# Kernel tuning notes

Hardware: AMD Instinct MI355X
Metric: run time of the kernel (lower is better)

The kernel has to match this reference:

```python
import jax, jax.numpy as jnp
import numpy as np

IN_DIM = 512
OUT_DIM = 512
KEY_DIM = 512
FILTER_LENGTH = 32
STRIDE = 4
B, T = 8, 2048


def setup_inputs() -> dict:
    key = jax.random.key(0)
    ks = jax.random.split(key, 7)
    s_in = 1.0 / np.sqrt(IN_DIM)
    x = jax.random.normal(ks[0], (B, T, IN_DIM), dtype=jnp.float32)
    Wq = jax.random.uniform(ks[1], (IN_DIM, KEY_DIM), jnp.float32, -s_in, s_in)
    bq = jax.random.uniform(ks[2], (KEY_DIM,), jnp.float32, -s_in, s_in)
    Wk = jax.random.uniform(ks[3], (IN_DIM, KEY_DIM), jnp.float32, -s_in, s_in)
    bk = jax.random.uniform(ks[4], (KEY_DIM,), jnp.float32, -s_in, s_in)
    Wv = jax.random.uniform(ks[5], (IN_DIM, OUT_DIM), jnp.float32, -s_in, s_in)
    bv = jax.random.uniform(ks[6], (OUT_DIM,), jnp.float32, -s_in, s_in)
    return {"x": x, "Wq": Wq, "bq": bq, "Wk": Wk, "bk": bk, "Wv": Wv, "bv": bv}


def reference(x, Wq, bq, Wk, bk, Wv, bv):
    # x: (B, T, in_dim)
    Bsz, T_, _ = x.shape
    F = FILTER_LENGTH
    T_out = (T_ - F) // STRIDE + 1
    starts = jnp.arange(T_out) * STRIDE                 # (T_out,)
    win_idx = starts[:, None] + jnp.arange(F)[None, :]  # (T_out, F)
    center_idx = starts + F // 2                        # (T_out,)

    q = x @ Wq + bq   # (B, T, key_dim)
    k = x @ Wk + bk   # (B, T, key_dim)
    v = x @ Wv + bv   # (B, T, out_dim)

    q_c = q[:, center_idx]    # (B, T_out, key_dim) query at window center
    k_w = k[:, win_idx]       # (B, T_out, F, key_dim)
    v_w = v[:, win_idx]       # (B, T_out, F, out_dim)

    scale = 1.0 / jnp.sqrt(jnp.asarray(KEY_DIM, dtype=q.dtype))
    scores = jnp.einsum('btd,btfd->btf', q_c, k_w) * scale  # (B, T_out, F)
    attn = jax.nn.softmax(scores, axis=-1)
    out = jnp.einsum('btf,btfd->btd', attn, v_w)            # (B, T_out, out_dim)
    return out
```

## Files before the change

### kernel.cpp

```cpp
#include <hip/hip_runtime.h>
#include <hip/hip_bf16.h>
#include <cstdint>

#define FLT 32
#define TOUT 505
#define TT 2048
#define MROWS 16384
#define QROWS 4040
#define KDIM 512
#define BK 64
#define NT 8

typedef float f32x4 __attribute__((ext_vector_type(4)));
typedef __bf16 bf16x8 __attribute__((ext_vector_type(8)));

static __device__ __forceinline__ ushort f2bf(float f) {
  uint32_t u = __float_as_uint(f);
  uint32_t r = (u + 0x7fffu + ((u >> 16) & 1u)) >> 16;
  return (ushort)r;
}
static __device__ __forceinline__ float bf2f(ushort h) {
  return __uint_as_float(((uint32_t)h) << 16);
}
static __device__ __forceinline__ void pack8(const float4& lo, const float4& hi, ushort* v8) {
  v8[0] = f2bf(lo.x); v8[1] = f2bf(lo.y); v8[2] = f2bf(lo.z); v8[3] = f2bf(lo.w);
  v8[4] = f2bf(hi.x); v8[5] = f2bf(hi.y); v8[6] = f2bf(hi.z); v8[7] = f2bf(hi.w);
}

__global__ void wprep_kernel(const float* __restrict__ Wq, const float* __restrict__ Wk,
                             const float* __restrict__ Wv, const float* __restrict__ bq,
                             const float* __restrict__ bk, const float* __restrict__ bv,
                             ushort* __restrict__ wt, float* __restrict__ bias) {
  const int bid = blockIdx.x;
  const int tid = threadIdx.x;
  if (bid < 192) {
    __shared__ ushort lds[64][66];
    int mat = bid >> 6;
    int w = bid & 63;
    int k0 = (w >> 3) * 64, n0 = (w & 7) * 64;
    const float* W = (mat == 0) ? Wq : (mat == 1) ? Wk : Wv;
    int nn = tid & 63;
    #pragma unroll
    for (int r = 0; r < 16; ++r) {
      int kk = r * 4 + (tid >> 6);
      lds[kk][nn] = f2bf(W[(size_t)(k0 + kk) * 512 + n0 + nn]);
    }
    __syncthreads();
    int kk2 = tid & 63;
    #pragma unroll
    for (int r = 0; r < 16; ++r) {
      int nn2 = r * 4 + (tid >> 6);
      wt[(size_t)(mat * 512 + n0 + nn2) * 512 + k0 + kk2] = lds[kk2][nn2];
    }
  } else {
    #pragma unroll
    for (int e = 0; e < 6; ++e) {
      int n = tid * 6 + e;
      const float* bsrc = (n < 512) ? bq : (n < 1024) ? bk : bv;
      bias[n] = bsrc[n & 511];
    }
  }
}

__global__ __launch_bounds__(256, 2) void gemm_kernel(
    const float* __restrict__ xf, const ushort* __restrict__ wt,
    const float* __restrict__ bias, ushort* __restrict__ kv, ushort* __restrict__ qc) {
  __shared__ char smem[33792];
  ushort* const As = (ushort*)smem;
  ushort* const Bs = (ushort*)(smem + 16384);

  const int tid = threadIdx.x;
  const int lane = tid & 63;
  const int wv = tid >> 6;
  const int bid = blockIdx.x;

  int m0, n0, ost, gather, mlim;
  const ushort* wtb;
  const float* biasb;
  ushort* outp;
  if (bid < 1024) {
    int swz = (bid & 7) * 128 + (bid >> 3);
    m0 = (swz >> 3) * 128; n0 = (swz & 7) * 128;
    wtb = wt + (size_t)512 * KDIM; biasb = bias + 512;
    outp = kv; ost = 1024; gather = 0; mlim = MROWS;
  } else {
    int b2 = bid - 1024;
    int swz = (b2 & 7) * 16 + (b2 >> 3);
    m0 = (swz >> 2) * 128; n0 = (swz & 3) * 128;
    wtb = wt; biasb = bias;
    outp = qc; ost = 512; gather = 1; mlim = QROWS;
  }

  const float* aF[4];
  uint aDst[4];
  const ushort* bS[4];
  #pragma unroll
  for (int i = 0; i < 4; ++i) {
    int idx = i * 4096 + tid * 16;
    int row = idx >> 7;
    int colb = idx & 127;
    aDst[i] = (uint)(row * 128 + (colb ^ ((row & 7) << 4)));
    int scol = (colb ^ ((row & 7) << 4)) >> 1;
    size_t arow;
    if (gather) {
      int r = m0 + row;
      if (r > QROWS - 1) r = QROWS - 1;
      int bb = r / TOUT;
      int t2 = r - bb * TOUT;
      arow = (size_t)bb * TT + (size_t)t2 * 4 + FLT / 2;
    } else {
      arow = (size_t)(m0 + row);
    }
    aF[i] = xf + arow * KDIM + (colb >> 1);
    bS[i] = wtb + (size_t)(n0 + row) * KDIM + scol;
  }

  const int fr = lane & 15;
  const int fq = lane >> 4;
  const int wr = wv >> 1;
  const int wc = wv & 1;

  f32x4 acc[4][4];
  #pragma unroll
  for (int i = 0; i < 4; ++i)
    #pragma unroll
    for (int j = 0; j < 4; ++j) acc[i][j] = (f32x4){0.f, 0.f, 0.f, 0.f};

  for (int t = 0; t < NT; ++t) {
    __syncthreads();
    const int koff = t * BK;
    #pragma unroll
    for (int i = 0; i < 4; ++i) {
      __builtin_amdgcn_global_load_lds(
          (const __attribute__((address_space(1))) unsigned int*)(bS[i] + koff),
          (__attribute__((address_space(3))) unsigned int*)((char*)Bs + i * 4096 + tid * 16),
          16, 0, 0);
    }
    #pragma unroll
    for (int i = 0; i < 4; ++i) {
      float4 lo = *reinterpret_cast<const float4*>(aF[i] + koff);
      float4 hi = *reinterpret_cast<const float4*>(aF[i] + koff + 4);
      ushort v8[8]; pack8(lo, hi, v8);
      *reinterpret_cast<uint4*>((char*)As + aDst[i]) = *reinterpret_cast<const uint4*>(v8);
    }
    __syncthreads();

    #pragma unroll
    for (int ks = 0; ks < 2; ++ks) {
      bf16x8 af[4], bg[4];
      #pragma unroll
      for (int i = 0; i < 4; ++i) {
        int ra = wr * 64 + i * 16 + fr;
        int ca = ks * 64 + fq * 16;
        af[i] = *reinterpret_cast<const bf16x8*>(
            (const char*)As + ra * 128 + (ca ^ ((ra & 7) << 4)));
        int rb = wc * 64 + i * 16 + fr;
        bg[i] = *reinterpret_cast<const bf16x8*>(
            (const char*)Bs + rb * 128 + (ca ^ ((rb & 7) << 4)));
      }
      #pragma unroll
      for (int i = 0; i < 4; ++i)
        #pragma unroll
        for (int j = 0; j < 4; ++j)
          acc[i][j] = __builtin_amdgcn_mfma_f32_16x16x32_bf16(af[i], bg[j], acc[i][j], 0, 0, 0);
    }
  }

  __syncthreads();
  ushort* const ep = (ushort*)smem;
  #pragma unroll
  for (int j = 0; j < 4; ++j) {
    int colg = n0 + wc * 64 + j * 16 + fr;
    int coll = wc * 64 + j * 16 + fr;
    float bvl = biasb[colg];
    #pragma unroll
    for (int i = 0; i < 4; ++i) {
      int rowl = wr * 64 + i * 16 + fq * 4;
      #pragma unroll
      for (int r = 0; r < 4; ++r)
        ep[(rowl + r) * 132 + coll] = f2bf(acc[i][j][r] + bvl);
    }
  }
  __syncthreads();
  #pragma unroll
  for (int it = 0; it < 8; ++it) {
    int row = it * 16 + (tid >> 4);
    int gr = m0 + row;
    if (gr < mlim) {
      uint4 val = *reinterpret_cast<const uint4*>(&ep[row * 132 + (tid & 15) * 8]);
      *reinterpret_cast<uint4*>(outp + (size_t)gr * ost + n0 + (tid & 15) * 8) = val;
    }
  }
}

__global__ __launch_bounds__(256) void attn_kernel(
    const ushort* __restrict__ kv,
    const ushort* __restrict__ qc,
    float* __restrict__ out) {
  __shared__ float q_lds[KDIM];
  __shared__ float s_lds[FLT];
  __shared__ float p_lds[FLT];

  const int bid = blockIdx.x;
  const int b = bid & 7;
  const int t = bid >> 3;
  const size_t base_row = (size_t)b * TT + (size_t)t * 4;
  const int tid = threadIdx.x;
  const int lane = tid & 63;
  const int wv = tid >> 6;

  {
    const ushort* qrow = qc + ((size_t)b * TOUT + t) * KDIM;
    uint v = *reinterpret_cast<const uint*>(qrow + tid * 2);
    q_lds[tid * 2]     = bf2f((ushort)(v & 0xffffu));
    q_lds[tid * 2 + 1] = bf2f((ushort)(v >> 16));
  }
  __syncthreads();

  const int fl = lane >> 3;
  const int f = wv * 8 + fl;
  const int sub = lane & 7;
  const ushort* krow = kv + (base_row + f) * 1024;
  float acc = 0.f;
  #pragma unroll
  for (int j = 0; j < 8; ++j) {
    int d = (j * 8 + sub) * 8;
    uint4 kv4 = *reinterpret_cast<const uint4*>(krow + d);
    const ushort* ks = reinterpret_cast<const ushort*>(&kv4);
    #pragma unroll
    for (int e = 0; e < 8; ++e) acc += q_lds[d + e] * bf2f(ks[e]);
  }
  acc += __shfl_xor(acc, 1);
  acc += __shfl_xor(acc, 2);
  acc += __shfl_xor(acc, 4);
  if (sub == 0) s_lds[f] = acc * 0.04419417382415922f;
  __syncthreads();

  float m = -1e30f;
  #pragma unroll
  for (int i = 0; i < FLT; ++i) m = fmaxf(m, s_lds[i]);
  if (tid < FLT) p_lds[tid] = __expf(s_lds[tid] - m);
  __syncthreads();
  float sum = 0.f;
  #pragma unroll
  for (int i = 0; i < FLT; ++i) sum += p_lds[i];
  const float inv = 1.f / sum;

  const int d = tid * 2;
  float o0 = 0.f, o1 = 0.f;
  const ushort* vbase = kv + base_row * 1024 + 512 + d;
  #pragma unroll
  for (int ff = 0; ff < FLT; ++ff) {
    uint vvv = *reinterpret_cast<const uint*>(vbase + (size_t)ff * 1024);
    float w = p_lds[ff] * inv;
    o0 += w * bf2f((ushort)(vvv & 0xffffu));
    o1 += w * bf2f((ushort)(vvv >> 16));
  }
  float2* op = reinterpret_cast<float2*>(out + ((size_t)b * TOUT + t) * 512 + d);
  *op = make_float2(o0, o1);
}

extern "C" void kernel_launch(void* const* d_in, const int* in_sizes, int n_in,
                              void* d_out, int out_size, void* d_ws, size_t ws_size,
                              hipStream_t stream) {
  const float* x  = (const float*)d_in[0];
  const float* Wq = (const float*)d_in[1];
  const float* bq = (const float*)d_in[2];
  const float* Wk = (const float*)d_in[3];
  const float* bk = (const float*)d_in[4];
  const float* Wv = (const float*)d_in[5];
  const float* bv = (const float*)d_in[6];
  float* out = (float*)d_out;

  char* ws = (char*)d_ws;
  ushort* wt   = (ushort*)ws;
  float*  bias = (float*)(ws + 1572864);
  ushort* kvb  = (ushort*)(ws + 1581056);
  ushort* qc   = (ushort*)(ws + 1581056 + 33554432);

  hipLaunchKernelGGL(wprep_kernel, dim3(193), dim3(256), 0, stream,
                     Wq, Wk, Wv, bq, bk, bv, wt, bias);
  hipLaunchKernelGGL(gemm_kernel, dim3(1152), dim3(256), 0, stream,
                     x, wt, bias, kvb, qc);
  hipLaunchKernelGGL(attn_kernel, dim3(QROWS), dim3(256), 0, stream, kvb, qc, out);
}
```

Measured before the change: 60.25 us.

## Load A fragments directly from global into registers, drop A LDS staging

The GEMM no longer stages the fp32-to-bf16 converted A tile in shared memory. Each wave loads its own A fragment straight from global memory into registers and converts it with native bf16 casts. The LDS-staged epilogue is replaced by direct scattered 2-byte global stores, and launch bounds are raised to allow more blocks per CU. This cuts LDS usage and sync work, but A rows are now re-read by both column waves, global A loads are less coalesced, and the output stores are narrow and uncoalesced.

```diff
diff --git a/kernel.cpp b/kernel.cpp
--- a/kernel.cpp
+++ b/kernel.cpp
@@ -22,9 +22,11 @@
 static __device__ __forceinline__ float bf2f(ushort h) {
   return __uint_as_float(((uint32_t)h) << 16);
 }
-static __device__ __forceinline__ void pack8(const float4& lo, const float4& hi, ushort* v8) {
-  v8[0] = f2bf(lo.x); v8[1] = f2bf(lo.y); v8[2] = f2bf(lo.z); v8[3] = f2bf(lo.w);
-  v8[4] = f2bf(hi.x); v8[5] = f2bf(hi.y); v8[6] = f2bf(hi.z); v8[7] = f2bf(hi.w);
+static __device__ __forceinline__ bf16x8 cvt8(const float4& lo, const float4& hi) {
+  bf16x8 v;
+  v[0] = (__bf16)lo.x; v[1] = (__bf16)lo.y; v[2] = (__bf16)lo.z; v[3] = (__bf16)lo.w;
+  v[4] = (__bf16)hi.x; v[5] = (__bf16)hi.y; v[6] = (__bf16)hi.z; v[7] = (__bf16)hi.w;
+  return v;
 }
 
 __global__ void wprep_kernel(const float* __restrict__ Wq, const float* __restrict__ Wk,
@@ -62,19 +64,17 @@
   }
 }
 
-__global__ __launch_bounds__(256, 2) void gemm_kernel(
+__global__ __launch_bounds__(256, 4) void gemm_kernel(
     const float* __restrict__ xf, const ushort* __restrict__ wt,
     const float* __restrict__ bias, ushort* __restrict__ kv, ushort* __restrict__ qc) {
-  __shared__ char smem[33792];
-  ushort* const As = (ushort*)smem;
-  ushort* const Bs = (ushort*)(smem + 16384);
+  __shared__ ushort Bs[128 * 64];
 
   const int tid = threadIdx.x;
   const int lane = tid & 63;
   const int wv = tid >> 6;
   const int bid = blockIdx.x;
 
-  int m0, n0, ost, gather, mlim;
+  int m0, n0, ost, gather;
   const ushort* wtb;
   const float* biasb;
   ushort* outp;
@@ -82,43 +82,45 @@
     int swz = (bid & 7) * 128 + (bid >> 3);
     m0 = (swz >> 3) * 128; n0 = (swz & 7) * 128;
     wtb = wt + (size_t)512 * KDIM; biasb = bias + 512;
-    outp = kv; ost = 1024; gather = 0; mlim = MROWS;
+    outp = kv; ost = 1024; gather = 0;
   } else {
     int b2 = bid - 1024;
     int swz = (b2 & 7) * 16 + (b2 >> 3);
     m0 = (swz >> 2) * 128; n0 = (swz & 3) * 128;
     wtb = wt; biasb = bias;
-    outp = qc; ost = 512; gather = 1; mlim = QROWS;
-  }
-
-  const float* aF[4];
-  uint aDst[4];
+    outp = qc; ost = 512; gather = 1;
+  }
+
   const ushort* bS[4];
   #pragma unroll
   for (int i = 0; i < 4; ++i) {
     int idx = i * 4096 + tid * 16;
     int row = idx >> 7;
     int colb = idx & 127;
-    aDst[i] = (uint)(row * 128 + (colb ^ ((row & 7) << 4)));
     int scol = (colb ^ ((row & 7) << 4)) >> 1;
+    bS[i] = wtb + (size_t)(n0 + row) * KDIM + scol;
+  }
+
+  const int fr = lane & 15;
+  const int fq = lane >> 4;
+  const int wr = wv >> 1;
+  const int wc = wv & 1;
+
+  const float* aP[4];
+  #pragma unroll
+  for (int i = 0; i < 4; ++i) {
+    int r = m0 + wr * 64 + i * 16 + fr;
     size_t arow;
     if (gather) {
-      int r = m0 + row;
       if (r > QROWS - 1) r = QROWS - 1;
       int bb = r / TOUT;
       int t2 = r - bb * TOUT;
       arow = (size_t)bb * TT + (size_t)t2 * 4 + FLT / 2;
     } else {
-      arow = (size_t)(m0 + row);
-    }
-    aF[i] = xf + arow * KDIM + (colb >> 1);
-    bS[i] = wtb + (size_t)(n0 + row) * KDIM + scol;
-  }
-
-  const int fr = lane & 15;
-  const int fq = lane >> 4;
-  const int wr = wv >> 1;
-  const int wc = wv & 1;
+      arow = (size_t)r;
+    }
+    aP[i] = xf + arow * KDIM;
+  }
 
   f32x4 acc[4][4];
   #pragma unroll
@@ -136,26 +138,24 @@
           (__attribute__((address_space(3))) unsigned int*)((char*)Bs + i * 4096 + tid * 16),
           16, 0, 0);
     }
-    #pragma unroll
-    for (int i = 0; i < 4; ++i) {
-      float4 lo = *reinterpret_cast<const float4*>(aF[i] + koff);
-      float4 hi = *reinterpret_cast<const float4*>(aF[i] + koff + 4);
-      ushort v8[8]; pack8(lo, hi, v8);
-      *reinterpret_cast<uint4*>((char*)As + aDst[i]) = *reinterpret_cast<const uint4*>(v8);
-    }
     __syncthreads();
 
     #pragma unroll
     for (int ks = 0; ks < 2; ++ks) {
-      bf16x8 af[4], bg[4];
+      bf16x8 af[4];
       #pragma unroll
       for (int i = 0; i < 4; ++i) {
-        int ra = wr * 64 + i * 16 + fr;
+        const float* p = aP[i] + koff + ks * 32 + fq * 8;
+        float4 lo = *reinterpret_cast<const float4*>(p);
+        float4 hi = *reinterpret_cast<const float4*>(p + 4);
+        af[i] = cvt8(lo, hi);
+      }
+      bf16x8 bg[4];
+      #pragma unroll
+      for (int j = 0; j < 4; ++j) {
+        int rb = wc * 64 + j * 16 + fr;
         int ca = ks * 64 + fq * 16;
-        af[i] = *reinterpret_cast<const bf16x8*>(
-            (const char*)As + ra * 128 + (ca ^ ((ra & 7) << 4)));
-        int rb = wc * 64 + i * 16 + fr;
-        bg[i] = *reinterpret_cast<const bf16x8*>(
+        bg[j] = *reinterpret_cast<const bf16x8*>(
             (const char*)Bs + rb * 128 + (ca ^ ((rb & 7) << 4)));
       }
       #pragma unroll
@@ -166,29 +166,18 @@
     }
   }
 
-  __syncthreads();
-  ushort* const ep = (ushort*)smem;
   #pragma unroll
   for (int j = 0; j < 4; ++j) {
-    int colg = n0 + wc * 64 + j * 16 + fr;
-    int coll = wc * 64 + j * 16 + fr;
-    float bvl = biasb[colg];
+    int col = n0 + wc * 64 + j * 16 + fr;
+    float bvl = biasb[col];
     #pragma unroll
     for (int i = 0; i < 4; ++i) {
-      int rowl = wr * 64 + i * 16 + fq * 4;
-      #pragma unroll
-      for (int r = 0; r < 4; ++r)
-        ep[(rowl + r) * 132 + coll] = f2bf(acc[i][j][r] + bvl);
-    }
-  }
-  __syncthreads();
-  #pragma unroll
-  for (int it = 0; it < 8; ++it) {
-    int row = it * 16 + (tid >> 4);
-    int gr = m0 + row;
-    if (gr < mlim) {
-      uint4 val = *reinterpret_cast<const uint4*>(&ep[row * 132 + (tid & 15) * 8]);
-      *reinterpret_cast<uint4*>(outp + (size_t)gr * ost + n0 + (tid & 15) * 8) = val;
+      int rowb = m0 + wr * 64 + i * 16 + fq * 4;
+      #pragma unroll
+      for (int r = 0; r < 4; ++r) {
+        if (!gather || (rowb + r) < QROWS)
+          outp[(size_t)(rowb + r) * ost + col] = f2bf(acc[i][j][r] + bvl);
+      }
     }
   }
 }
```

Result: slower. 136.5 us (+126.5%).

## Apply attention weights to x and project with Wv afterwards; drop key bias

Applied to the files above, without the earlier changes.

Since the softmax weights sum to one, attn·(xWv+bv) equals (attn·x)Wv+bv, so V is no longer materialised for all rows. The key bias is dropped because it shifts every score in a window by the same amount and cancels in softmax. The attention kernel now stages a bf16 window of x in LDS for 8 consecutive outputs and writes a weighted-x buffer, and a new small GEMM applies Wv plus bias. This removes the large V projection and the K/V writes, at the cost of an extra kernel launch, fewer and larger attention blocks (512 instead of 4040), and an extra bf16 rounding of the intermediate.

```diff
diff --git a/kernel.cpp b/kernel.cpp
--- a/kernel.cpp
+++ b/kernel.cpp
@@ -28,43 +28,32 @@
 }
 
 __global__ void wprep_kernel(const float* __restrict__ Wq, const float* __restrict__ Wk,
-                             const float* __restrict__ Wv, const float* __restrict__ bq,
-                             const float* __restrict__ bk, const float* __restrict__ bv,
-                             ushort* __restrict__ wt, float* __restrict__ bias) {
+                             const float* __restrict__ Wv, ushort* __restrict__ wt) {
   const int bid = blockIdx.x;
   const int tid = threadIdx.x;
-  if (bid < 192) {
-    __shared__ ushort lds[64][66];
-    int mat = bid >> 6;
-    int w = bid & 63;
-    int k0 = (w >> 3) * 64, n0 = (w & 7) * 64;
-    const float* W = (mat == 0) ? Wq : (mat == 1) ? Wk : Wv;
-    int nn = tid & 63;
-    #pragma unroll
-    for (int r = 0; r < 16; ++r) {
-      int kk = r * 4 + (tid >> 6);
-      lds[kk][nn] = f2bf(W[(size_t)(k0 + kk) * 512 + n0 + nn]);
-    }
-    __syncthreads();
-    int kk2 = tid & 63;
-    #pragma unroll
-    for (int r = 0; r < 16; ++r) {
-      int nn2 = r * 4 + (tid >> 6);
-      wt[(size_t)(mat * 512 + n0 + nn2) * 512 + k0 + kk2] = lds[kk2][nn2];
-    }
-  } else {
-    #pragma unroll
-    for (int e = 0; e < 6; ++e) {
-      int n = tid * 6 + e;
-      const float* bsrc = (n < 512) ? bq : (n < 1024) ? bk : bv;
-      bias[n] = bsrc[n & 511];
-    }
+  __shared__ ushort lds[64][66];
+  int mat = bid >> 6;
+  int w = bid & 63;
+  int k0 = (w >> 3) * 64, n0 = (w & 7) * 64;
+  const float* W = (mat == 0) ? Wq : (mat == 1) ? Wk : Wv;
+  int nn = tid & 63;
+  #pragma unroll
+  for (int r = 0; r < 16; ++r) {
+    int kk = r * 4 + (tid >> 6);
+    lds[kk][nn] = f2bf(W[(size_t)(k0 + kk) * 512 + n0 + nn]);
+  }
+  __syncthreads();
+  int kk2 = tid & 63;
+  #pragma unroll
+  for (int r = 0; r < 16; ++r) {
+    int nn2 = r * 4 + (tid >> 6);
+    wt[(size_t)(mat * 512 + n0 + nn2) * 512 + k0 + kk2] = lds[kk2][nn2];
   }
 }
 
 __global__ __launch_bounds__(256, 2) void gemm_kernel(
     const float* __restrict__ xf, const ushort* __restrict__ wt,
-    const float* __restrict__ bias, ushort* __restrict__ kv, ushort* __restrict__ qc) {
+    const float* __restrict__ bq, ushort* __restrict__ kb, ushort* __restrict__ qc) {
   __shared__ char smem[33792];
   ushort* const As = (ushort*)smem;
   ushort* const Bs = (ushort*)(smem + 16384);
@@ -74,21 +63,20 @@
   const int wv = tid >> 6;
   const int bid = blockIdx.x;
 
-  int m0, n0, ost, gather, mlim;
+  int m0, n0, gather, mlim;
   const ushort* wtb;
-  const float* biasb;
   ushort* outp;
-  if (bid < 1024) {
-    int swz = (bid & 7) * 128 + (bid >> 3);
-    m0 = (swz >> 3) * 128; n0 = (swz & 7) * 128;
-    wtb = wt + (size_t)512 * KDIM; biasb = bias + 512;
-    outp = kv; ost = 1024; gather = 0; mlim = MROWS;
+  if (bid < 512) {
+    int swz = (bid & 7) * 64 + (bid >> 3);
+    m0 = (swz >> 2) * 128; n0 = (swz & 3) * 128;
+    wtb = wt + (size_t)512 * KDIM;
+    outp = kb; gather = 0; mlim = MROWS;
   } else {
-    int b2 = bid - 1024;
+    int b2 = bid - 512;
     int swz = (b2 & 7) * 16 + (b2 >> 3);
     m0 = (swz >> 2) * 128; n0 = (swz & 3) * 128;
-    wtb = wt; biasb = bias;
-    outp = qc; ost = 512; gather = 1; mlim = QROWS;
+    wtb = wt;
+    outp = qc; gather = 1; mlim = QROWS;
   }
 
   const float* aF[4];
@@ -170,9 +158,9 @@
   ushort* const ep = (ushort*)smem;
   #pragma unroll
   for (int j = 0; j < 4; ++j) {
-    int colg = n0 + wc * 64 + j * 16 + fr;
+    int col = n0 + wc * 64 + j * 16 + fr;
     int coll = wc * 64 + j * 16 + fr;
-    float bvl = biasb[colg];
+    float bvl = gather ? bq[col] : 0.f;
     #pragma unroll
     for (int i = 0; i < 4; ++i) {
       int rowl = wr * 64 + i * 16 + fq * 4;
@@ -188,76 +176,190 @@
     int gr = m0 + row;
     if (gr < mlim) {
       uint4 val = *reinterpret_cast<const uint4*>(&ep[row * 132 + (tid & 15) * 8]);
-      *reinterpret_cast<uint4*>(outp + (size_t)gr * ost + n0 + (tid & 15) * 8) = val;
+      *reinterpret_cast<uint4*>(outp + (size_t)gr * 512 + n0 + (tid & 15) * 8) = val;
     }
   }
 }
 
 __global__ __launch_bounds__(256) void attn_kernel(
-    const ushort* __restrict__ kv,
+    const float* __restrict__ xf,
+    const ushort* __restrict__ kb,
     const ushort* __restrict__ qc,
-    float* __restrict__ out) {
-  __shared__ float q_lds[KDIM];
+    ushort* __restrict__ ubuf) {
+  __shared__ char xw[61440];
+  __shared__ float q_lds[512];
   __shared__ float s_lds[FLT];
   __shared__ float p_lds[FLT];
 
   const int bid = blockIdx.x;
   const int b = bid & 7;
-  const int t = bid >> 3;
-  const size_t base_row = (size_t)b * TT + (size_t)t * 4;
+  const int g = bid >> 3;
+  const int t0 = g * 8;
+  const int nt = min(8, TOUT - t0);
+  const int rows = 4 * (nt - 1) + 32;
+  const size_t base_row = (size_t)b * TT + (size_t)t0 * 4;
   const int tid = threadIdx.x;
   const int lane = tid & 63;
   const int wv = tid >> 6;
 
-  {
-    const ushort* qrow = qc + ((size_t)b * TOUT + t) * KDIM;
-    uint v = *reinterpret_cast<const uint*>(qrow + tid * 2);
-    q_lds[tid * 2]     = bf2f((ushort)(v & 0xffffu));
-    q_lds[tid * 2 + 1] = bf2f((ushort)(v >> 16));
-  }
-  __syncthreads();
-
-  const int fl = lane >> 3;
-  const int f = wv * 8 + fl;
-  const int sub = lane & 7;
-  const ushort* krow = kv + (base_row + f) * 1024;
-  float acc = 0.f;
-  #pragma unroll
-  for (int j = 0; j < 8; ++j) {
-    int d = (j * 8 + sub) * 8;
-    uint4 kv4 = *reinterpret_cast<const uint4*>(krow + d);
-    const ushort* ks = reinterpret_cast<const ushort*>(&kv4);
-    #pragma unroll
-    for (int e = 0; e < 8; ++e) acc += q_lds[d + e] * bf2f(ks[e]);
-  }
-  acc += __shfl_xor(acc, 1);
-  acc += __shfl_xor(acc, 2);
-  acc += __shfl_xor(acc, 4);
-  if (sub == 0) s_lds[f] = acc * 0.04419417382415922f;
-  __syncthreads();
-
-  float m = -1e30f;
-  #pragma unroll
-  for (int i = 0; i < FLT; ++i) m = fmaxf(m, s_lds[i]);
-  if (tid < FLT) p_lds[tid] = __expf(s_lds[tid] - m);
-  __syncthreads();
-  float sum = 0.f;
-  #pragma unroll
-  for (int i = 0; i < FLT; ++i) sum += p_lds[i];
-  const float inv = 1.f / sum;
-
-  const int d = tid * 2;
-  float o0 = 0.f, o1 = 0.f;
-  const ushort* vbase = kv + base_row * 1024 + 512 + d;
-  #pragma unroll
-  for (int ff = 0; ff < FLT; ++ff) {
-    uint vvv = *reinterpret_cast<const uint*>(vbase + (size_t)ff * 1024);
-    float w = p_lds[ff] * inv;
-    o0 += w * bf2f((ushort)(vvv & 0xffffu));
-    o1 += w * bf2f((ushort)(vvv >> 16));
-  }
-  float2* op = reinterpret_cast<float2*>(out + ((size_t)b * TOUT + t) * 512 + d);
-  *op = make_float2(o0, o1);
+  #pragma unroll
+  for (int i = 0; i < 15; ++i) {
+    int gi = i * 2048 + tid * 8;
+    int row = gi >> 9;
+    int col = gi & 511;
+    if (row < rows) {
+      const float* src = xf + (base_row + row) * 512 + col;
+      float4 lo = *reinterpret_cast<const float4*>(src);
+      float4 hi = *reinterpret_cast<const float4*>(src + 4);
+      ushort v8[8]; pack8(lo, hi, v8);
+      *reinterpret_cast<uint4*>(xw + row * 1024 + ((2 * col) ^ ((row & 7) << 4))) =
+          *reinterpret_cast<const uint4*>(v8);
+    }
+  }
+
+  for (int tt = 0; tt < nt; ++tt) {
+    {
+      uint v = *reinterpret_cast<const uint*>(
+          qc + ((size_t)b * TOUT + t0 + tt) * 512 + tid * 2);
+      q_lds[tid * 2]     = bf2f((ushort)(v & 0xffffu));
+      q_lds[tid * 2 + 1] = bf2f((ushort)(v >> 16));
+    }
+    __syncthreads();
+
+    const int f = wv * 8 + (lane >> 3);
+    const int sub = lane & 7;
+    const ushort* krow = kb + (base_row + (size_t)(4 * tt + f)) * 512;
+    float acc = 0.f;
+    #pragma unroll
+    for (int j = 0; j < 8; ++j) {
+      int d = (j * 8 + sub) * 8;
+      uint4 kv4 = *reinterpret_cast<const uint4*>(krow + d);
+      const ushort* ks = reinterpret_cast<const ushort*>(&kv4);
+      #pragma unroll
+      for (int e = 0; e < 8; ++e) acc += q_lds[d + e] * bf2f(ks[e]);
+    }
+    acc += __shfl_xor(acc, 1);
+    acc += __shfl_xor(acc, 2);
+    acc += __shfl_xor(acc, 4);
+    if (sub == 0) s_lds[f] = acc * 0.04419417382415922f;
+    __syncthreads();
+
+    float m = -1e30f;
+    #pragma unroll
+    for (int i2 = 0; i2 < FLT; ++i2) m = fmaxf(m, s_lds[i2]);
+    if (tid < FLT) p_lds[tid] = __expf(s_lds[tid] - m);
+    __syncthreads();
+    float sum = 0.f;
+    #pragma unroll
+    for (int i2 = 0; i2 < FLT; ++i2) sum += p_lds[i2];
+    const float inv = 1.f / sum;
+
+    const int d = tid * 2;
+    float o0 = 0.f, o1 = 0.f;
+    #pragma unroll
+    for (int ff = 0; ff < FLT; ++ff) {
+      int r2 = 4 * tt + ff;
+      uint vv = *reinterpret_cast<const uint*>(
+          xw + r2 * 1024 + ((2 * d) ^ ((r2 & 7) << 4)));
+      float w = p_lds[ff] * inv;
+      o0 += w * bf2f((ushort)(vv & 0xffffu));
+      o1 += w * bf2f((ushort)(vv >> 16));
+    }
+    uint pk = ((uint)f2bf(o1) << 16) | (uint)f2bf(o0);
+    *reinterpret_cast<uint*>(ubuf + ((size_t)b * TOUT + t0 + tt) * 512 + d) = pk;
+    __syncthreads();
+  }
+}
+
+__global__ __launch_bounds__(256, 2) void ogemm_kernel(
+    const ushort* __restrict__ ubuf, const ushort* __restrict__ wvt,
+    const float* __restrict__ bv, float* __restrict__ out) {
+  __shared__ ushort As[128 * 64];
+  __shared__ ushort Bs[128 * 64];
+
+  const int tid = threadIdx.x;
+  const int lane = tid & 63;
+  const int wv = tid >> 6;
+  const int swz = (blockIdx.x & 7) * 16 + (blockIdx.x >> 3);
+  const int m0 = (swz >> 2) * 128;
+  const int n0 = (swz & 3) * 128;
+
+  const ushort* aS[4];
+  const ushort* bS[4];
+  #pragma unroll
+  for (int i = 0; i < 4; ++i) {
+    int idx = i * 4096 + tid * 16;
+    int row = idx >> 7;
+    int colb = idx & 127;
+    int scol = (colb ^ ((row & 7) << 4)) >> 1;
+    int r = m0 + row; if (r > QROWS - 1) r = QROWS - 1;
+    aS[i] = ubuf + (size_t)r * KDIM + scol;
+    bS[i] = wvt + (size_t)(n0 + row) * KDIM + scol;
+  }
+
+  const int fr = lane & 15;
+  const int fq = lane >> 4;
+  const int wr = wv >> 1;
+  const int wc = wv & 1;
+
+  f32x4 acc[4][4];
+  #pragma unroll
+  for (int i = 0; i < 4; ++i)
+    #pragma unroll
+    for (int j = 0; j < 4; ++j) acc[i][j] = (f32x4){0.f, 0.f, 0.f, 0.f};
+
+  for (int t = 0; t < NT; ++t) {
+    __syncthreads();
+    const int koff = t * BK;
+    #pragma unroll
+    for (int i = 0; i < 4; ++i) {
+      int ldst = i * 4096 + tid * 16;
+      __builtin_amdgcn_global_load_lds(
+          (const __attribute__((address_space(1))) unsigned int*)(aS[i] + koff),
+          (__attribute__((address_space(3))) unsigned int*)((char*)As + ldst),
+          16, 0, 0);
+      __builtin_amdgcn_global_load_lds(
+          (const __attribute__((address_space(1))) unsigned int*)(bS[i] + koff),
+          (__attribute__((address_space(3))) unsigned int*)((char*)Bs + ldst),
+          16, 0, 0);
+    }
+    __syncthreads();
+
+    #pragma unroll
+    for (int ks = 0; ks < 2; ++ks) {
+      bf16x8 af[4], bg[4];
+      #pragma unroll
+      for (int i = 0; i < 4; ++i) {
+        int ra = wr * 64 + i * 16 + fr;
+        int ca = ks * 64 + fq * 16;
+        af[i] = *reinterpret_cast<const bf16x8*>(
+            (const char*)As + ra * 128 + (ca ^ ((ra & 7) << 4)));
+        int rb = wc * 64 + i * 16 + fr;
+        bg[i] = *reinterpret_cast<const bf16x8*>(
+            (const char*)Bs + rb * 128 + (ca ^ ((rb & 7) << 4)));
+      }
+      #pragma unroll
+      for (int i = 0; i < 4; ++i)
+        #pragma unroll
+        for (int j = 0; j < 4; ++j)
+          acc[i][j] = __builtin_amdgcn_mfma_f32_16x16x32_bf16(af[i], bg[j], acc[i][j], 0, 0, 0);
+    }
+  }
+
+  #pragma unroll
+  for (int j = 0; j < 4; ++j) {
+    int col = n0 + wc * 64 + j * 16 + fr;
+    float bvl = bv[col];
+    #pragma unroll
+    for (int i = 0; i < 4; ++i) {
+      int rowb = m0 + wr * 64 + i * 16 + fq * 4;
+      #pragma unroll
+      for (int r = 0; r < 4; ++r) {
+        if (rowb + r < QROWS)
+          out[(size_t)(rowb + r) * 512 + col] = acc[i][j][r] + bvl;
+      }
+    }
+  }
 }
 
 extern "C" void kernel_launch(void* const* d_in, const int* in_sizes, int n_in,
@@ -267,20 +369,21 @@
   const float* Wq = (const float*)d_in[1];
   const float* bq = (const float*)d_in[2];
   const float* Wk = (const float*)d_in[3];
-  const float* bk = (const float*)d_in[4];
   const float* Wv = (const float*)d_in[5];
   const float* bv = (const float*)d_in[6];
   float* out = (float*)d_out;
 
   char* ws = (char*)d_ws;
   ushort* wt   = (ushort*)ws;
-  float*  bias = (float*)(ws + 1572864);
-  ushort* kvb  = (ushort*)(ws + 1581056);
-  ushort* qc   = (ushort*)(ws + 1581056 + 33554432);
-
-  hipLaunchKernelGGL(wprep_kernel, dim3(193), dim3(256), 0, stream,
-                     Wq, Wk, Wv, bq, bk, bv, wt, bias);
-  hipLaunchKernelGGL(gemm_kernel, dim3(1152), dim3(256), 0, stream,
-                     x, wt, bias, kvb, qc);
-  hipLaunchKernelGGL(attn_kernel, dim3(QROWS), dim3(256), 0, stream, kvb, qc, out);
-}
+  ushort* kb   = (ushort*)(ws + 1572864);
+  ushort* qc   = (ushort*)(ws + 1572864 + 16777216);
+  ushort* ubuf = (ushort*)(ws + 1572864 + 16777216 + 4194304);
+
+  hipLaunchKernelGGL(wprep_kernel, dim3(192), dim3(256), 0, stream, Wq, Wk, Wv, wt);
+  hipLaunchKernelGGL(gemm_kernel, dim3(640), dim3(256), 0, stream,
+                     x, wt, bq, kb, qc);
+  hipLaunchKernelGGL(attn_kernel, dim3(512), dim3(256), 0, stream,
+                     x, kb, qc, ubuf);
+  hipLaunchKernelGGL(ogemm_kernel, dim3(128), dim3(256), 0, stream,
+                     ubuf, wt + (size_t)1024 * 512, bv, out);
+}
```

Result: slower. 74.35 us (+23.4%).

## Widen GEMM tile to 128x256 with 8 waves and drop LDS epilogue staging

Applied to the files above, without the earlier changes.

The projection GEMM now uses 512-thread blocks computing 128x256 output tiles, halving the block count and the number of times the fp32 activation tile is loaded and converted to bf16 per output column. The epilogue no longer stages results through LDS for coalesced 16-byte stores; each lane writes scalar bf16 values directly to global memory. This trades fewer redundant A loads against less coalesced output stores and larger per-block LDS use, which may reduce occupancy.

```diff
diff --git a/kernel.cpp b/kernel.cpp
--- a/kernel.cpp
+++ b/kernel.cpp
@@ -62,45 +62,45 @@
   }
 }
 
-__global__ __launch_bounds__(256, 2) void gemm_kernel(
+__global__ __launch_bounds__(512, 2) void gemm_kernel(
     const float* __restrict__ xf, const ushort* __restrict__ wt,
     const float* __restrict__ bias, ushort* __restrict__ kv, ushort* __restrict__ qc) {
-  __shared__ char smem[33792];
-  ushort* const As = (ushort*)smem;
-  ushort* const Bs = (ushort*)(smem + 16384);
+  __shared__ char smem[49152];
+  char* const As = smem;
+  char* const Bs = smem + 16384;
 
   const int tid = threadIdx.x;
   const int lane = tid & 63;
   const int wv = tid >> 6;
+  const int wr = wv >> 2;
+  const int wc = wv & 3;
   const int bid = blockIdx.x;
 
   int m0, n0, ost, gather, mlim;
   const ushort* wtb;
   const float* biasb;
   ushort* outp;
-  if (bid < 1024) {
-    int swz = (bid & 7) * 128 + (bid >> 3);
-    m0 = (swz >> 3) * 128; n0 = (swz & 7) * 128;
+  if (bid < 512) {
+    int swz = (bid & 7) * 64 + (bid >> 3);
+    m0 = (swz >> 2) * 128; n0 = (swz & 3) * 256;
     wtb = wt + (size_t)512 * KDIM; biasb = bias + 512;
     outp = kv; ost = 1024; gather = 0; mlim = MROWS;
   } else {
-    int b2 = bid - 1024;
-    int swz = (b2 & 7) * 16 + (b2 >> 3);
-    m0 = (swz >> 2) * 128; n0 = (swz & 3) * 128;
+    int l2 = bid - 512;
+    int swz = (l2 & 7) * 8 + (l2 >> 3);
+    m0 = (swz >> 1) * 128; n0 = (swz & 1) * 256;
     wtb = wt; biasb = bias;
     outp = qc; ost = 512; gather = 1; mlim = QROWS;
   }
 
-  const float* aF[4];
-  uint aDst[4];
-  const ushort* bS[4];
-  #pragma unroll
-  for (int i = 0; i < 4; ++i) {
-    int idx = i * 4096 + tid * 16;
+  const float* aF[2];
+  uint aDst[2];
+  #pragma unroll
+  for (int i = 0; i < 2; ++i) {
+    int idx = i * 8192 + tid * 16;
     int row = idx >> 7;
     int colb = idx & 127;
     aDst[i] = (uint)(row * 128 + (colb ^ ((row & 7) << 4)));
-    int scol = (colb ^ ((row & 7) << 4)) >> 1;
     size_t arow;
     if (gather) {
       int r = m0 + row;
@@ -112,13 +112,19 @@
       arow = (size_t)(m0 + row);
     }
     aF[i] = xf + arow * KDIM + (colb >> 1);
+  }
+  const ushort* bS[4];
+  #pragma unroll
+  for (int i = 0; i < 4; ++i) {
+    int idx = i * 8192 + tid * 16;
+    int row = idx >> 7;
+    int colb = idx & 127;
+    int scol = (colb ^ ((row & 7) << 4)) >> 1;
     bS[i] = wtb + (size_t)(n0 + row) * KDIM + scol;
   }
 
   const int fr = lane & 15;
   const int fq = lane >> 4;
-  const int wr = wv >> 1;
-  const int wc = wv & 1;
 
   f32x4 acc[4][4];
   #pragma unroll
@@ -133,30 +139,28 @@
     for (int i = 0; i < 4; ++i) {
       __builtin_amdgcn_global_load_lds(
           (const __attribute__((address_space(1))) unsigned int*)(bS[i] + koff),
-          (__attribute__((address_space(3))) unsigned int*)((char*)Bs + i * 4096 + tid * 16),
+          (__attribute__((address_space(3))) unsigned int*)(Bs + i * 8192 + tid * 16),
           16, 0, 0);
     }
     #pragma unroll
-    for (int i = 0; i < 4; ++i) {
+    for (int i = 0; i < 2; ++i) {
       float4 lo = *reinterpret_cast<const float4*>(aF[i] + koff);
       float4 hi = *reinterpret_cast<const float4*>(aF[i] + koff + 4);
       ushort v8[8]; pack8(lo, hi, v8);
-      *reinterpret_cast<uint4*>((char*)As + aDst[i]) = *reinterpret_cast<const uint4*>(v8);
+      *reinterpret_cast<uint4*>(As + aDst[i]) = *reinterpret_cast<const uint4*>(v8);
     }
     __syncthreads();
 
     #pragma unroll
     for (int ks = 0; ks < 2; ++ks) {
+      const int cab = ks * 64 + fq * 16;
       bf16x8 af[4], bg[4];
       #pragma unroll
       for (int i = 0; i < 4; ++i) {
         int ra = wr * 64 + i * 16 + fr;
-        int ca = ks * 64 + fq * 16;
-        af[i] = *reinterpret_cast<const bf16x8*>(
-            (const char*)As + ra * 128 + (ca ^ ((ra & 7) << 4)));
+        af[i] = *reinterpret_cast<const bf16x8*>(As + ra * 128 + (cab ^ ((ra & 7) << 4)));
         int rb = wc * 64 + i * 16 + fr;
-        bg[i] = *reinterpret_cast<const bf16x8*>(
-            (const char*)Bs + rb * 128 + (ca ^ ((rb & 7) << 4)));
+        bg[i] = *reinterpret_cast<const bf16x8*>(Bs + rb * 128 + (cab ^ ((rb & 7) << 4)));
       }
       #pragma unroll
       for (int i = 0; i < 4; ++i)
@@ -166,29 +170,18 @@
     }
   }
 
-  __syncthreads();
-  ushort* const ep = (ushort*)smem;
   #pragma unroll
   for (int j = 0; j < 4; ++j) {
-    int colg = n0 + wc * 64 + j * 16 + fr;
-    int coll = wc * 64 + j * 16 + fr;
-    float bvl = biasb[colg];
+    int col = n0 + wc * 64 + j * 16 + fr;
+    float bvl = biasb[col];
     #pragma unroll
     for (int i = 0; i < 4; ++i) {
-      int rowl = wr * 64 + i * 16 + fq * 4;
+      int rowb = m0 + wr * 64 + i * 16 + fq * 4;
       #pragma unroll
-      for (int r = 0; r < 4; ++r)
-        ep[(rowl + r) * 132 + coll] = f2bf(acc[i][j][r] + bvl);
-    }
-  }
-  __syncthreads();
-  #pragma unroll
-  for (int it = 0; it < 8; ++it) {
-    int row = it * 16 + (tid >> 4);
-    int gr = m0 + row;
-    if (gr < mlim) {
-      uint4 val = *reinterpret_cast<const uint4*>(&ep[row * 132 + (tid & 15) * 8]);
-      *reinterpret_cast<uint4*>(outp + (size_t)gr * ost + n0 + (tid & 15) * 8) = val;
+      for (int r = 0; r < 4; ++r) {
+        if (!gather || (rowb + r) < mlim)
+          outp[(size_t)(rowb + r) * ost + col] = f2bf(acc[i][j][r] + bvl);
+      }
     }
   }
 }
@@ -280,7 +273,7 @@
 
   hipLaunchKernelGGL(wprep_kernel, dim3(193), dim3(256), 0, stream,
                      Wq, Wk, Wv, bq, bk, bv, wt, bias);
-  hipLaunchKernelGGL(gemm_kernel, dim3(1152), dim3(256), 0, stream,
+  hipLaunchKernelGGL(gemm_kernel, dim3(576), dim3(512), 0, stream,
                      x, wt, bias, kvb, qc);
   hipLaunchKernelGGL(attn_kernel, dim3(QROWS), dim3(256), 0, stream, kvb, qc, out);
 }
```

Result: slower. 76.24 us (+26.5%).
